# Kernel tuning notes

Hardware: AMD Instinct MI355X
Metric: run time of the kernel (lower is better)

Reference implementation:

```python
import jax, jax.numpy as jnp
import numpy as np

SCALE = 0.5
DROP_P = 0.2

def setup_inputs() -> dict:
    key = jax.random.key(0)
    k1, k2 = jax.random.split(key)
    x1 = jax.random.normal(k1, (8, 2048, 128), dtype=jnp.float32)
    x2 = jax.random.normal(k2, (8, 2048, 128), dtype=jnp.float32)
    return {"x1": x1, "x2": x2}

def reference(x1, x2):
    # scores: [B, M, N] = x1 @ x2^T, scaled by 0.5
    scores = jnp.einsum('bmd,bnd->bmn', x1, x2) * SCALE
    probs = jax.nn.softmax(scores, axis=-1)
    # dropout p=0.2 (training mode in the torch source); fixed key for determinism
    keep = jax.random.bernoulli(jax.random.key(42), 1.0 - DROP_P, probs.shape)
    probs = jnp.where(keep, probs / (1.0 - DROP_P), 0.0)
    # out: [B, M, D] = probs @ x2
    return jnp.einsum('bmn,bnd->bmd', probs, x2)
```

## Files before the change

kernel.cpp:

```cpp
#include <hip/hip_runtime.h>
#include <stdint.h>


typedef __bf16 bf16x8 __attribute__((ext_vector_type(8)));
typedef float f32x4 __attribute__((ext_vector_type(4)));

union FragAB {
  bf16x8 v;
  uint32_t u[4];
};

__device__ __forceinline__ uint32_t rotl32(uint32_t x, uint32_t r) {
  return (x << r) | (x >> (32u - r));
}

__device__ __forceinline__ void threefry2x32_k42(uint32_t in0, uint32_t in1,
                                                 uint32_t& o0, uint32_t& o1) {
  const uint32_t ks0 = 0u;
  const uint32_t ks1 = 42u;
  const uint32_t ks2 = 0x1BD11BDAu ^ 0u ^ 42u;
  uint32_t x0 = in0 + ks0;
  uint32_t x1 = in1 + ks1;
#define TFR(r) { x0 += x1; x1 = rotl32(x1, r); x1 ^= x0; }
  TFR(13u) TFR(15u) TFR(26u) TFR(6u)
  x0 += ks1; x1 += ks2 + 1u;
  TFR(17u) TFR(29u) TFR(16u) TFR(24u)
  x0 += ks2; x1 += ks0 + 2u;
  TFR(13u) TFR(15u) TFR(26u) TFR(6u)
  x0 += ks0; x1 += ks1 + 3u;
  TFR(17u) TFR(29u) TFR(16u) TFR(24u)
  x0 += ks1; x1 += ks2 + 4u;
  TFR(13u) TFR(15u) TFR(26u) TFR(6u)
  x0 += ks2; x1 += ks0 + 5u;
#undef TFR
  o0 = x0; o1 = x1;
}

__device__ __forceinline__ uint32_t pack_bf16(float a, float b) {
  __bf16 ba = (__bf16)a;
  __bf16 bb = (__bf16)b;
  uint32_t ua = (uint32_t)__builtin_bit_cast(uint16_t, ba);
  uint32_t ub = (uint32_t)__builtin_bit_cast(uint16_t, bb);
  return ua | (ub << 16);
}

#define KEEP_LT 3435974144u
#define MBIAS 40.0f

__launch_bounds__(256, 2)
__global__ void attn_kernel(const float* __restrict__ x1,
                            const float* __restrict__ x2,
                            float* __restrict__ out) {
  __shared__ __attribute__((aligned(16))) uint32_t SMEM[4][4800];

  const int tid = threadIdx.x;
  const int wv = __builtin_amdgcn_readfirstlane(tid >> 6);
  const int lane = tid & 63;
  const int l15 = lane & 15;
  const int g = lane >> 4;
  const int b = blockIdx.y;
  const int m0 = blockIdx.x * 32;

  uint32_t* KtW = &SMEM[wv][0];
  uint32_t* VtW = &SMEM[wv][2176];
  uint32_t* PbW = &SMEM[wv][4480];

  const float QSCALE = 0.5f * 1.44269504088896340736f;
  FragAB qf[2][4];
  #pragma unroll
  for (int s = 0; s < 2; ++s) {
    const float* qp_base = x1 + ((size_t)b * 2048 + m0 + s * 16 + l15) * 128;
    #pragma unroll
    for (int c = 0; c < 4; ++c) {
      const float* qp = qp_base + c * 32 + g * 8;
      float4 f0 = *(const float4*)(qp);
      float4 f1 = *(const float4*)(qp + 4);
      qf[s][c].u[0] = pack_bf16(f0.x * QSCALE, f0.y * QSCALE);
      qf[s][c].u[1] = pack_bf16(f0.z * QSCALE, f0.w * QSCALE);
      qf[s][c].u[2] = pack_bf16(f1.x * QSCALE, f1.y * QSCALE);
      qf[s][c].u[3] = pack_bf16(f1.z * QSCALE, f1.w * QSCALE);
    }
  }

  f32x4 o[2][8];
  #pragma unroll
  for (int s = 0; s < 2; ++s)
    #pragma unroll
    for (int dt = 0; dt < 8; ++dt) o[s][dt] = (f32x4){0.f, 0.f, 0.f, 0.f};
  float lsum[2] = {0.f, 0.f};

  uint32_t rb[2];
  #pragma unroll
  for (int s = 0; s < 2; ++s)
    rb[s] = (uint32_t)b * 4194304u +
            (uint32_t)(m0 + s * 16 + l15) * 2048u + (uint32_t)(wv * 512);

  const float4* x2b4 = (const float4*)(x2 + (size_t)b * 2048 * 128);
  const uint32_t permsel = (l15 & 1) ? 0x07060302u : 0x05040100u;

  for (int tile = 0; tile < 16; ++tile) {
    const int n0g = wv * 512 + tile * 32;

    #pragma unroll
    for (int i = 0; i < 16; ++i) {
      int n = 2 * i + (lane >> 5);
      int dq = lane & 31;
      float4 v = x2b4[(size_t)(n0g + n) * 32 + dq];
      uint32_t p0 = pack_bf16(v.x, v.y);
      uint32_t p1 = pack_bf16(v.z, v.w);
      *(uint2*)&KtW[n * 68 + 2 * dq] = make_uint2(p0, p1);
      VtW[dq * 36 + n] = p0;
      VtW[(dq + 32) * 36 + n] = p1;
    }
    asm volatile("s_waitcnt lgkmcnt(0)" ::: "memory");

    f32x4 sa[2][2];
    #pragma unroll
    for (int s = 0; s < 2; ++s)
      #pragma unroll
      for (int t = 0; t < 2; ++t) sa[s][t] = (f32x4){0.f, 0.f, 0.f, 0.f};
    #pragma unroll
    for (int c = 0; c < 4; ++c) {
      FragAB k0, k1;
      uint4 a0 = *(const uint4*)&KtW[l15 * 68 + c * 16 + 4 * g];
      uint4 a1 = *(const uint4*)&KtW[(16 + l15) * 68 + c * 16 + 4 * g];
      k0.u[0] = a0.x; k0.u[1] = a0.y; k0.u[2] = a0.z; k0.u[3] = a0.w;
      k1.u[0] = a1.x; k1.u[1] = a1.y; k1.u[2] = a1.z; k1.u[3] = a1.w;
      sa[0][0] = __builtin_amdgcn_mfma_f32_16x16x32_bf16(k0.v, qf[0][c].v, sa[0][0], 0, 0, 0);
      sa[0][1] = __builtin_amdgcn_mfma_f32_16x16x32_bf16(k1.v, qf[0][c].v, sa[0][1], 0, 0, 0);
      sa[1][0] = __builtin_amdgcn_mfma_f32_16x16x32_bf16(k0.v, qf[1][c].v, sa[1][0], 0, 0, 0);
      sa[1][1] = __builtin_amdgcn_mfma_f32_16x16x32_bf16(k1.v, qf[1][c].v, sa[1][1], 0, 0, 0);
    }

    FragAB pa[2];
    #pragma unroll
    for (int s = 0; s < 2; ++s) {
      #pragma unroll
      for (int t = 0; t < 2; ++t) {
        float p0 = __builtin_amdgcn_exp2f(sa[s][t][0] - MBIAS);
        float p1 = __builtin_amdgcn_exp2f(sa[s][t][1] - MBIAS);
        float p2 = __builtin_amdgcn_exp2f(sa[s][t][2] - MBIAS);
        float p3 = __builtin_amdgcn_exp2f(sa[s][t][3] - MBIAS);
        lsum[s] += (p0 + p1) + (p2 + p3);
        uint32_t ib = rb[s] + (uint32_t)(tile * 32 + t * 16 + 4 * g);
        uint32_t h0, h1, bits;
        threefry2x32_k42(0u, ib + 0u, h0, h1); bits = h0 ^ h1;
        float q0 = (bits < KEEP_LT) ? p0 : 0.0f;
        threefry2x32_k42(0u, ib + 1u, h0, h1); bits = h0 ^ h1;
        float q1 = (bits < KEEP_LT) ? p1 : 0.0f;
        threefry2x32_k42(0u, ib + 2u, h0, h1); bits = h0 ^ h1;
        float q2 = (bits < KEEP_LT) ? p2 : 0.0f;
        threefry2x32_k42(0u, ib + 3u, h0, h1); bits = h0 ^ h1;
        float q3 = (bits < KEEP_LT) ? p3 : 0.0f;
        *(uint2*)&PbW[l15 * 20 + t * 8 + 2 * g] =
            make_uint2(pack_bf16(q0, q1), pack_bf16(q2, q3));
      }
      asm volatile("s_waitcnt lgkmcnt(0)" ::: "memory");
      uint4 pu = *(const uint4*)&PbW[l15 * 20 + 4 * g];
      pa[s].u[0] = pu.x; pa[s].u[1] = pu.y; pa[s].u[2] = pu.z; pa[s].u[3] = pu.w;
    }

    #pragma unroll
    for (int dt = 0; dt < 8; ++dt) {
      int rowp = ((l15 >> 1) & 1) * 32 + 4 * dt + (l15 >> 2);
      const uint32_t* vr = &VtW[rowp * 36 + 8 * g];
      uint4 U0 = *(const uint4*)vr;
      uint4 U1 = *(const uint4*)(vr + 4);
      FragAB vb;
      vb.u[0] = __builtin_amdgcn_perm(U0.y, U0.x, permsel);
      vb.u[1] = __builtin_amdgcn_perm(U0.w, U0.z, permsel);
      vb.u[2] = __builtin_amdgcn_perm(U1.y, U1.x, permsel);
      vb.u[3] = __builtin_amdgcn_perm(U1.w, U1.z, permsel);
      o[0][dt] = __builtin_amdgcn_mfma_f32_16x16x32_bf16(pa[0].v, vb.v, o[0][dt], 0, 0, 0);
      o[1][dt] = __builtin_amdgcn_mfma_f32_16x16x32_bf16(pa[1].v, vb.v, o[1][dt], 0, 0, 0);
    }
  }

  __syncthreads();
  float* EP = (float*)&SMEM[0][0];
  #pragma unroll
  for (int s = 0; s < 2; ++s) {
    #pragma unroll
    for (int dt = 0; dt < 8; ++dt)
      #pragma unroll
      for (int r = 0; r < 4; ++r)
        EP[(((wv * 2 + s) * 8 + dt) * 4 + r) * 64 + lane] = o[s][dt][r];
    EP[16384 + (s * 16 + l15) * 16 + wv * 4 + g] = lsum[s];
  }
  __syncthreads();
  const int s = wv >> 1;
  float scale[4];
  #pragma unroll
  for (int r = 0; r < 4; ++r) {
    const float4* lp = (const float4*)&EP[16384 + (s * 16 + 4 * g + r) * 16];
    float4 A = lp[0], B4 = lp[1], C4 = lp[2], D4 = lp[3];
    float L = ((A.x + A.y) + (A.z + A.w)) + ((B4.x + B4.y) + (B4.z + B4.w)) +
              ((C4.x + C4.y) + (C4.z + C4.w)) + ((D4.x + D4.y) + (D4.z + D4.w));
    scale[r] = 1.0f / (L * 0.8f);
  }
  #pragma unroll
  for (int it = 0; it < 4; ++it) {
    int dt = (wv * 4 + it) & 7;
    #pragma unroll
    for (int r = 0; r < 4; ++r) {
      int base = ((s * 8 + dt) * 4 + r) * 64 + lane;
      float tot = EP[base] + EP[base + 4096] + EP[base + 8192] + EP[base + 12288];
      out[((size_t)b * 2048 + m0 + s * 16 + 4 * g + r) * 128 + dt * 16 + l15] =
          tot * scale[r];
    }
  }
}

extern "C" void kernel_launch(void* const* d_in, const int* in_sizes, int n_in,
                              void* d_out, int out_size, void* d_ws, size_t ws_size,
                              hipStream_t stream) {
  const float* x1 = (const float*)d_in[0];
  const float* x2 = (const float*)d_in[1];
  float* out = (float*)d_out;
  dim3 grid(64, 8, 1);
  dim3 block(256, 1, 1);
  attn_kernel<<<grid, block, 0, stream>>>(x1, x2, out);
}
```

Measured before the change: 155.6 us.

## Halve query rows per block, load K directly from global, raise occupancy

Each block now handles 16 query rows instead of 32, doubling the grid and raising launch bounds to 4 blocks per CU. The K tile is no longer staged in LDS; each wave loads K rows straight from global memory into MFMA fragments. This shrinks LDS use and lets V use a tighter stride. The rotate in the threefry RNG is replaced by alignbit. In exchange, K/V global traffic per query row doubles and the per-tile RNG work is no longer amortized across two query slices.

```diff
diff --git a/kernel.cpp b/kernel.cpp
--- a/kernel.cpp
+++ b/kernel.cpp
@@ -10,9 +10,7 @@
   uint32_t u[4];
 };
 
-__device__ __forceinline__ uint32_t rotl32(uint32_t x, uint32_t r) {
-  return (x << r) | (x >> (32u - r));
-}
+#define ROTL(x, r) __builtin_amdgcn_alignbit((x), (x), 32u - (r))
 
 __device__ __forceinline__ void threefry2x32_k42(uint32_t in0, uint32_t in1,
                                                  uint32_t& o0, uint32_t& o1) {
@@ -21,7 +19,7 @@
   const uint32_t ks2 = 0x1BD11BDAu ^ 0u ^ 42u;
   uint32_t x0 = in0 + ks0;
   uint32_t x1 = in1 + ks1;
-#define TFR(r) { x0 += x1; x1 = rotl32(x1, r); x1 ^= x0; }
+#define TFR(r) { x0 += x1; x1 = ROTL(x1, r); x1 ^= x0; }
   TFR(13u) TFR(15u) TFR(26u) TFR(6u)
   x0 += ks1; x1 += ks2 + 1u;
   TFR(17u) TFR(29u) TFR(16u) TFR(24u)
@@ -47,11 +45,11 @@
 #define KEEP_LT 3435974144u
 #define MBIAS 40.0f
 
-__launch_bounds__(256, 2)
+__launch_bounds__(256, 4)
 __global__ void attn_kernel(const float* __restrict__ x1,
                             const float* __restrict__ x2,
                             float* __restrict__ out) {
-  __shared__ __attribute__((aligned(16))) uint32_t SMEM[4][4800];
+  __shared__ __attribute__((aligned(16))) uint32_t SMEM[4][2496];
 
   const int tid = threadIdx.x;
   const int wv = __builtin_amdgcn_readfirstlane(tid >> 6);
@@ -59,153 +57,143 @@
   const int l15 = lane & 15;
   const int g = lane >> 4;
   const int b = blockIdx.y;
-  const int m0 = blockIdx.x * 32;
-
-  uint32_t* KtW = &SMEM[wv][0];
-  uint32_t* VtW = &SMEM[wv][2176];
-  uint32_t* PbW = &SMEM[wv][4480];
+  const int m0 = blockIdx.x * 16;
+
+  uint32_t* VtW = &SMEM[wv][0];
+  uint32_t* PbW = &SMEM[wv][2176];
+
+  const float* x2b = x2 + (size_t)b * 2048 * 128;
+  const float4* x2b4 = (const float4*)x2b;
 
   const float QSCALE = 0.5f * 1.44269504088896340736f;
-  FragAB qf[2][4];
-  #pragma unroll
-  for (int s = 0; s < 2; ++s) {
-    const float* qp_base = x1 + ((size_t)b * 2048 + m0 + s * 16 + l15) * 128;
+  FragAB qf[4];
+  {
+    const float* qp_base = x1 + ((size_t)b * 2048 + m0 + l15) * 128;
     #pragma unroll
     for (int c = 0; c < 4; ++c) {
       const float* qp = qp_base + c * 32 + g * 8;
       float4 f0 = *(const float4*)(qp);
       float4 f1 = *(const float4*)(qp + 4);
-      qf[s][c].u[0] = pack_bf16(f0.x * QSCALE, f0.y * QSCALE);
-      qf[s][c].u[1] = pack_bf16(f0.z * QSCALE, f0.w * QSCALE);
-      qf[s][c].u[2] = pack_bf16(f1.x * QSCALE, f1.y * QSCALE);
-      qf[s][c].u[3] = pack_bf16(f1.z * QSCALE, f1.w * QSCALE);
-    }
-  }
-
-  f32x4 o[2][8];
-  #pragma unroll
-  for (int s = 0; s < 2; ++s)
-    #pragma unroll
-    for (int dt = 0; dt < 8; ++dt) o[s][dt] = (f32x4){0.f, 0.f, 0.f, 0.f};
-  float lsum[2] = {0.f, 0.f};
-
-  uint32_t rb[2];
-  #pragma unroll
-  for (int s = 0; s < 2; ++s)
-    rb[s] = (uint32_t)b * 4194304u +
-            (uint32_t)(m0 + s * 16 + l15) * 2048u + (uint32_t)(wv * 512);
-
-  const float4* x2b4 = (const float4*)(x2 + (size_t)b * 2048 * 128);
+      qf[c].u[0] = pack_bf16(f0.x * QSCALE, f0.y * QSCALE);
+      qf[c].u[1] = pack_bf16(f0.z * QSCALE, f0.w * QSCALE);
+      qf[c].u[2] = pack_bf16(f1.x * QSCALE, f1.y * QSCALE);
+      qf[c].u[3] = pack_bf16(f1.z * QSCALE, f1.w * QSCALE);
+    }
+  }
+
+  f32x4 o[8];
+  #pragma unroll
+  for (int dt = 0; dt < 8; ++dt) o[dt] = (f32x4){0.f, 0.f, 0.f, 0.f};
+  float lsum = 0.f;
+
+  const uint32_t rb = (uint32_t)b * 4194304u +
+                      (uint32_t)(m0 + l15) * 2048u + (uint32_t)(wv * 512);
+
   const uint32_t permsel = (l15 & 1) ? 0x07060302u : 0x05040100u;
+  const int nrow = lane >> 5;
+  const int dq = lane & 31;
 
   for (int tile = 0; tile < 16; ++tile) {
     const int n0g = wv * 512 + tile * 32;
 
     #pragma unroll
     for (int i = 0; i < 16; ++i) {
-      int n = 2 * i + (lane >> 5);
-      int dq = lane & 31;
+      int n = 2 * i + nrow;
       float4 v = x2b4[(size_t)(n0g + n) * 32 + dq];
-      uint32_t p0 = pack_bf16(v.x, v.y);
-      uint32_t p1 = pack_bf16(v.z, v.w);
-      *(uint2*)&KtW[n * 68 + 2 * dq] = make_uint2(p0, p1);
-      VtW[dq * 36 + n] = p0;
-      VtW[(dq + 32) * 36 + n] = p1;
+      VtW[dq * 34 + n] = pack_bf16(v.x, v.y);
+      VtW[(dq + 32) * 34 + n] = pack_bf16(v.z, v.w);
+    }
+
+    f32x4 sa[2];
+    #pragma unroll
+    for (int t = 0; t < 2; ++t) sa[t] = (f32x4){0.f, 0.f, 0.f, 0.f};
+    #pragma unroll
+    for (int t = 0; t < 2; ++t) {
+      const float* krow = x2b + (size_t)(n0g + t * 16 + l15) * 128 + g * 8;
+      #pragma unroll
+      for (int c = 0; c < 4; ++c) {
+        float4 f0 = *(const float4*)(krow + c * 32);
+        float4 f1 = *(const float4*)(krow + c * 32 + 4);
+        FragAB kf;
+        kf.u[0] = pack_bf16(f0.x, f0.y);
+        kf.u[1] = pack_bf16(f0.z, f0.w);
+        kf.u[2] = pack_bf16(f1.x, f1.y);
+        kf.u[3] = pack_bf16(f1.z, f1.w);
+        sa[t] = __builtin_amdgcn_mfma_f32_16x16x32_bf16(kf.v, qf[c].v, sa[t], 0, 0, 0);
+      }
+    }
+
+    #pragma unroll
+    for (int t = 0; t < 2; ++t) {
+      float p0 = __builtin_amdgcn_exp2f(sa[t][0] - MBIAS);
+      float p1 = __builtin_amdgcn_exp2f(sa[t][1] - MBIAS);
+      float p2 = __builtin_amdgcn_exp2f(sa[t][2] - MBIAS);
+      float p3 = __builtin_amdgcn_exp2f(sa[t][3] - MBIAS);
+      lsum += (p0 + p1) + (p2 + p3);
+      uint32_t ib = rb + (uint32_t)(tile * 32 + t * 16 + 4 * g);
+      uint32_t h0, h1, bits;
+      threefry2x32_k42(0u, ib + 0u, h0, h1); bits = h0 ^ h1;
+      float q0 = (bits < KEEP_LT) ? p0 : 0.0f;
+      threefry2x32_k42(0u, ib + 1u, h0, h1); bits = h0 ^ h1;
+      float q1 = (bits < KEEP_LT) ? p1 : 0.0f;
+      threefry2x32_k42(0u, ib + 2u, h0, h1); bits = h0 ^ h1;
+      float q2 = (bits < KEEP_LT) ? p2 : 0.0f;
+      threefry2x32_k42(0u, ib + 3u, h0, h1); bits = h0 ^ h1;
+      float q3 = (bits < KEEP_LT) ? p3 : 0.0f;
+      *(uint2*)&PbW[l15 * 20 + t * 8 + 2 * g] =
+          make_uint2(pack_bf16(q0, q1), pack_bf16(q2, q3));
     }
     asm volatile("s_waitcnt lgkmcnt(0)" ::: "memory");
 
-    f32x4 sa[2][2];
-    #pragma unroll
-    for (int s = 0; s < 2; ++s)
-      #pragma unroll
-      for (int t = 0; t < 2; ++t) sa[s][t] = (f32x4){0.f, 0.f, 0.f, 0.f};
-    #pragma unroll
-    for (int c = 0; c < 4; ++c) {
-      FragAB k0, k1;
-      uint4 a0 = *(const uint4*)&KtW[l15 * 68 + c * 16 + 4 * g];
-      uint4 a1 = *(const uint4*)&KtW[(16 + l15) * 68 + c * 16 + 4 * g];
-      k0.u[0] = a0.x; k0.u[1] = a0.y; k0.u[2] = a0.z; k0.u[3] = a0.w;
-      k1.u[0] = a1.x; k1.u[1] = a1.y; k1.u[2] = a1.z; k1.u[3] = a1.w;
-      sa[0][0] = __builtin_amdgcn_mfma_f32_16x16x32_bf16(k0.v, qf[0][c].v, sa[0][0], 0, 0, 0);
-      sa[0][1] = __builtin_amdgcn_mfma_f32_16x16x32_bf16(k1.v, qf[0][c].v, sa[0][1], 0, 0, 0);
-      sa[1][0] = __builtin_amdgcn_mfma_f32_16x16x32_bf16(k0.v, qf[1][c].v, sa[1][0], 0, 0, 0);
-      sa[1][1] = __builtin_amdgcn_mfma_f32_16x16x32_bf16(k1.v, qf[1][c].v, sa[1][1], 0, 0, 0);
-    }
-
-    FragAB pa[2];
-    #pragma unroll
-    for (int s = 0; s < 2; ++s) {
-      #pragma unroll
-      for (int t = 0; t < 2; ++t) {
-        float p0 = __builtin_amdgcn_exp2f(sa[s][t][0] - MBIAS);
-        float p1 = __builtin_amdgcn_exp2f(sa[s][t][1] - MBIAS);
-        float p2 = __builtin_amdgcn_exp2f(sa[s][t][2] - MBIAS);
-        float p3 = __builtin_amdgcn_exp2f(sa[s][t][3] - MBIAS);
-        lsum[s] += (p0 + p1) + (p2 + p3);
-        uint32_t ib = rb[s] + (uint32_t)(tile * 32 + t * 16 + 4 * g);
-        uint32_t h0, h1, bits;
-        threefry2x32_k42(0u, ib + 0u, h0, h1); bits = h0 ^ h1;
-        float q0 = (bits < KEEP_LT) ? p0 : 0.0f;
-        threefry2x32_k42(0u, ib + 1u, h0, h1); bits = h0 ^ h1;
-        float q1 = (bits < KEEP_LT) ? p1 : 0.0f;
-        threefry2x32_k42(0u, ib + 2u, h0, h1); bits = h0 ^ h1;
-        float q2 = (bits < KEEP_LT) ? p2 : 0.0f;
-        threefry2x32_k42(0u, ib + 3u, h0, h1); bits = h0 ^ h1;
-        float q3 = (bits < KEEP_LT) ? p3 : 0.0f;
-        *(uint2*)&PbW[l15 * 20 + t * 8 + 2 * g] =
-            make_uint2(pack_bf16(q0, q1), pack_bf16(q2, q3));
-      }
-      asm volatile("s_waitcnt lgkmcnt(0)" ::: "memory");
+    FragAB pa;
+    {
       uint4 pu = *(const uint4*)&PbW[l15 * 20 + 4 * g];
-      pa[s].u[0] = pu.x; pa[s].u[1] = pu.y; pa[s].u[2] = pu.z; pa[s].u[3] = pu.w;
-    }
-
+      pa.u[0] = pu.x; pa.u[1] = pu.y; pa.u[2] = pu.z; pa.u[3] = pu.w;
+    }
     #pragma unroll
     for (int dt = 0; dt < 8; ++dt) {
       int rowp = ((l15 >> 1) & 1) * 32 + 4 * dt + (l15 >> 2);
-      const uint32_t* vr = &VtW[rowp * 36 + 8 * g];
-      uint4 U0 = *(const uint4*)vr;
-      uint4 U1 = *(const uint4*)(vr + 4);
+      const uint32_t* vr = &VtW[rowp * 34 + 8 * g];
+      uint2 w0 = *(const uint2*)(vr);
+      uint2 w1 = *(const uint2*)(vr + 2);
+      uint2 w2 = *(const uint2*)(vr + 4);
+      uint2 w3 = *(const uint2*)(vr + 6);
       FragAB vb;
-      vb.u[0] = __builtin_amdgcn_perm(U0.y, U0.x, permsel);
-      vb.u[1] = __builtin_amdgcn_perm(U0.w, U0.z, permsel);
-      vb.u[2] = __builtin_amdgcn_perm(U1.y, U1.x, permsel);
-      vb.u[3] = __builtin_amdgcn_perm(U1.w, U1.z, permsel);
-      o[0][dt] = __builtin_amdgcn_mfma_f32_16x16x32_bf16(pa[0].v, vb.v, o[0][dt], 0, 0, 0);
-      o[1][dt] = __builtin_amdgcn_mfma_f32_16x16x32_bf16(pa[1].v, vb.v, o[1][dt], 0, 0, 0);
+      vb.u[0] = __builtin_amdgcn_perm(w0.y, w0.x, permsel);
+      vb.u[1] = __builtin_amdgcn_perm(w1.y, w1.x, permsel);
+      vb.u[2] = __builtin_amdgcn_perm(w2.y, w2.x, permsel);
+      vb.u[3] = __builtin_amdgcn_perm(w3.y, w3.x, permsel);
+      o[dt] = __builtin_amdgcn_mfma_f32_16x16x32_bf16(pa.v, vb.v, o[dt], 0, 0, 0);
     }
   }
 
   __syncthreads();
   float* EP = (float*)&SMEM[0][0];
   #pragma unroll
-  for (int s = 0; s < 2; ++s) {
-    #pragma unroll
-    for (int dt = 0; dt < 8; ++dt)
-      #pragma unroll
-      for (int r = 0; r < 4; ++r)
-        EP[(((wv * 2 + s) * 8 + dt) * 4 + r) * 64 + lane] = o[s][dt][r];
-    EP[16384 + (s * 16 + l15) * 16 + wv * 4 + g] = lsum[s];
-  }
+  for (int dt = 0; dt < 8; ++dt)
+    #pragma unroll
+    for (int r = 0; r < 4; ++r)
+      EP[((wv * 8 + dt) * 4 + r) * 64 + lane] = o[dt][r];
+  EP[8192 + l15 * 16 + wv * 4 + g] = lsum;
   __syncthreads();
-  const int s = wv >> 1;
+
   float scale[4];
   #pragma unroll
   for (int r = 0; r < 4; ++r) {
-    const float4* lp = (const float4*)&EP[16384 + (s * 16 + 4 * g + r) * 16];
+    const float4* lp = (const float4*)&EP[8192 + (4 * g + r) * 16];
     float4 A = lp[0], B4 = lp[1], C4 = lp[2], D4 = lp[3];
     float L = ((A.x + A.y) + (A.z + A.w)) + ((B4.x + B4.y) + (B4.z + B4.w)) +
               ((C4.x + C4.y) + (C4.z + C4.w)) + ((D4.x + D4.y) + (D4.z + D4.w));
     scale[r] = 1.0f / (L * 0.8f);
   }
   #pragma unroll
-  for (int it = 0; it < 4; ++it) {
-    int dt = (wv * 4 + it) & 7;
+  for (int it = 0; it < 2; ++it) {
+    int dt = wv * 2 + it;
     #pragma unroll
     for (int r = 0; r < 4; ++r) {
-      int base = ((s * 8 + dt) * 4 + r) * 64 + lane;
-      float tot = EP[base] + EP[base + 4096] + EP[base + 8192] + EP[base + 12288];
-      out[((size_t)b * 2048 + m0 + s * 16 + 4 * g + r) * 128 + dt * 16 + l15] =
+      int base = (dt * 4 + r) * 64 + lane;
+      float tot = EP[base] + EP[base + 2048] + EP[base + 4096] + EP[base + 6144];
+      out[((size_t)b * 2048 + m0 + 4 * g + r) * 128 + dt * 16 + l15] =
           tot * scale[r];
     }
   }
@@ -217,7 +205,7 @@
   const float* x1 = (const float*)d_in[0];
   const float* x2 = (const float*)d_in[1];
   float* out = (float*)d_out;
-  dim3 grid(64, 8, 1);
+  dim3 grid(128, 8, 1);
   dim3 block(256, 1, 1);
   attn_kernel<<<grid, block, 0, stream>>>(x1, x2, out);
 }
```

Result: slower. 269.7 us (+73.3%).

## Precompute dropout masks into LDS and shrink shared memory footprint

Applied to the files above, without the earlier changes.

Threefry dropout bits are now computed in a prologue and packed into per-lane bitmasks in LDS, so the main tile loop only tests bits. Rotation uses alignbit. The K staging buffer is halved by processing the 32-key tile in two 16-row halves, and V and P paddings are tightened. The epilogue is reduced one row-group at a time, which cuts total LDS to allow more resident blocks. The cost is extra prologue latency and possible bank conflicts from the new strides.

```diff
diff --git a/kernel.cpp b/kernel.cpp
--- a/kernel.cpp
+++ b/kernel.cpp
@@ -10,9 +10,7 @@
   uint32_t u[4];
 };
 
-__device__ __forceinline__ uint32_t rotl32(uint32_t x, uint32_t r) {
-  return (x << r) | (x >> (32u - r));
-}
+#define ROTL(x, r) __builtin_amdgcn_alignbit((x), (x), 32u - (r))
 
 __device__ __forceinline__ void threefry2x32_k42(uint32_t in0, uint32_t in1,
                                                  uint32_t& o0, uint32_t& o1) {
@@ -21,7 +19,7 @@
   const uint32_t ks2 = 0x1BD11BDAu ^ 0u ^ 42u;
   uint32_t x0 = in0 + ks0;
   uint32_t x1 = in1 + ks1;
-#define TFR(r) { x0 += x1; x1 = rotl32(x1, r); x1 ^= x0; }
+#define TFR(r) { x0 += x1; x1 = ROTL(x1, r); x1 ^= x0; }
   TFR(13u) TFR(15u) TFR(26u) TFR(6u)
   x0 += ks1; x1 += ks2 + 1u;
   TFR(17u) TFR(29u) TFR(16u) TFR(24u)
@@ -36,6 +34,8 @@
   o0 = x0; o1 = x1;
 }
 
+#define KEEP_LT 3435974144u
+
 __device__ __forceinline__ uint32_t pack_bf16(float a, float b) {
   __bf16 ba = (__bf16)a;
   __bf16 bb = (__bf16)b;
@@ -44,14 +44,13 @@
   return ua | (ub << 16);
 }
 
-#define KEEP_LT 3435974144u
 #define MBIAS 40.0f
 
 __launch_bounds__(256, 2)
 __global__ void attn_kernel(const float* __restrict__ x1,
                             const float* __restrict__ x2,
                             float* __restrict__ out) {
-  __shared__ __attribute__((aligned(16))) uint32_t SMEM[4][4800];
+  __shared__ __attribute__((aligned(16))) uint32_t SMEM[4][4032];
 
   const int tid = threadIdx.x;
   const int wv = __builtin_amdgcn_readfirstlane(tid >> 6);
@@ -62,8 +61,38 @@
   const int m0 = blockIdx.x * 32;
 
   uint32_t* KtW = &SMEM[wv][0];
-  uint32_t* VtW = &SMEM[wv][2176];
-  uint32_t* PbW = &SMEM[wv][4480];
+  uint32_t* VtW = &SMEM[wv][1088];
+  uint32_t* PbW = &SMEM[wv][3264];
+  uint32_t* MkW = &SMEM[wv][3520];
+
+  uint32_t rb[2];
+  #pragma unroll
+  for (int s = 0; s < 2; ++s)
+    rb[s] = (uint32_t)b * 4194304u +
+            (uint32_t)(m0 + s * 16 + l15) * 2048u + (uint32_t)(wv * 512);
+
+  {
+    uint32_t accw = 0;
+    #pragma unroll 1
+    for (int t = 0; t < 16; ++t) {
+      uint32_t cur = 0;
+      #pragma unroll
+      for (int s = 0; s < 2; ++s) {
+        #pragma unroll
+        for (int t2 = 0; t2 < 2; ++t2) {
+          uint32_t ib = rb[s] + (uint32_t)(t * 32 + t2 * 16 + 4 * g);
+          #pragma unroll
+          for (int r = 0; r < 4; ++r) {
+            uint32_t h0, h1;
+            threefry2x32_k42(0u, ib + (uint32_t)r, h0, h1);
+            cur |= (((h0 ^ h1) < KEEP_LT) ? 1u : 0u) << (s * 8 + t2 * 4 + r);
+          }
+        }
+      }
+      if (t & 1) MkW[(t >> 1) * 64 + lane] = accw | (cur << 16);
+      else accw = cur;
+    }
+  }
 
   const float QSCALE = 0.5f * 1.44269504088896340736f;
   FragAB qf[2][4];
@@ -89,47 +118,48 @@
     for (int dt = 0; dt < 8; ++dt) o[s][dt] = (f32x4){0.f, 0.f, 0.f, 0.f};
   float lsum[2] = {0.f, 0.f};
 
-  uint32_t rb[2];
-  #pragma unroll
-  for (int s = 0; s < 2; ++s)
-    rb[s] = (uint32_t)b * 4194304u +
-            (uint32_t)(m0 + s * 16 + l15) * 2048u + (uint32_t)(wv * 512);
-
   const float4* x2b4 = (const float4*)(x2 + (size_t)b * 2048 * 128);
   const uint32_t permsel = (l15 & 1) ? 0x07060302u : 0x05040100u;
-
+  const int nrow = lane >> 5;
+  const int dq = lane & 31;
+
+  uint32_t mwreg = 0;
+
+  #pragma unroll 1
   for (int tile = 0; tile < 16; ++tile) {
     const int n0g = wv * 512 + tile * 32;
 
-    #pragma unroll
-    for (int i = 0; i < 16; ++i) {
-      int n = 2 * i + (lane >> 5);
-      int dq = lane & 31;
-      float4 v = x2b4[(size_t)(n0g + n) * 32 + dq];
-      uint32_t p0 = pack_bf16(v.x, v.y);
-      uint32_t p1 = pack_bf16(v.z, v.w);
-      *(uint2*)&KtW[n * 68 + 2 * dq] = make_uint2(p0, p1);
-      VtW[dq * 36 + n] = p0;
-      VtW[(dq + 32) * 36 + n] = p1;
-    }
-    asm volatile("s_waitcnt lgkmcnt(0)" ::: "memory");
+    if ((tile & 1) == 0)
+      mwreg = MkW[(tile >> 1) * 64 + lane];
+    const uint32_t mhalf = (tile & 1) ? (mwreg >> 16) : (mwreg & 0xFFFFu);
 
     f32x4 sa[2][2];
     #pragma unroll
     for (int s = 0; s < 2; ++s)
       #pragma unroll
       for (int t = 0; t < 2; ++t) sa[s][t] = (f32x4){0.f, 0.f, 0.f, 0.f};
-    #pragma unroll
-    for (int c = 0; c < 4; ++c) {
-      FragAB k0, k1;
-      uint4 a0 = *(const uint4*)&KtW[l15 * 68 + c * 16 + 4 * g];
-      uint4 a1 = *(const uint4*)&KtW[(16 + l15) * 68 + c * 16 + 4 * g];
-      k0.u[0] = a0.x; k0.u[1] = a0.y; k0.u[2] = a0.z; k0.u[3] = a0.w;
-      k1.u[0] = a1.x; k1.u[1] = a1.y; k1.u[2] = a1.z; k1.u[3] = a1.w;
-      sa[0][0] = __builtin_amdgcn_mfma_f32_16x16x32_bf16(k0.v, qf[0][c].v, sa[0][0], 0, 0, 0);
-      sa[0][1] = __builtin_amdgcn_mfma_f32_16x16x32_bf16(k1.v, qf[0][c].v, sa[0][1], 0, 0, 0);
-      sa[1][0] = __builtin_amdgcn_mfma_f32_16x16x32_bf16(k0.v, qf[1][c].v, sa[1][0], 0, 0, 0);
-      sa[1][1] = __builtin_amdgcn_mfma_f32_16x16x32_bf16(k1.v, qf[1][c].v, sa[1][1], 0, 0, 0);
+
+    #pragma unroll
+    for (int h = 0; h < 2; ++h) {
+      #pragma unroll
+      for (int i = 0; i < 8; ++i) {
+        int n = h * 16 + 2 * i + nrow;
+        float4 v = x2b4[(size_t)(n0g + n) * 32 + dq];
+        uint32_t p0 = pack_bf16(v.x, v.y);
+        uint32_t p1 = pack_bf16(v.z, v.w);
+        *(uint2*)&KtW[(2 * i + nrow) * 68 + 2 * dq] = make_uint2(p0, p1);
+        VtW[dq * 34 + n] = p0;
+        VtW[(dq + 32) * 34 + n] = p1;
+      }
+      asm volatile("s_waitcnt lgkmcnt(0)" ::: "memory");
+      #pragma unroll
+      for (int c = 0; c < 4; ++c) {
+        FragAB kf;
+        uint4 kk = *(const uint4*)&KtW[l15 * 68 + c * 16 + 4 * g];
+        kf.u[0] = kk.x; kf.u[1] = kk.y; kf.u[2] = kk.z; kf.u[3] = kk.w;
+        sa[0][h] = __builtin_amdgcn_mfma_f32_16x16x32_bf16(kf.v, qf[0][c].v, sa[0][h], 0, 0, 0);
+        sa[1][h] = __builtin_amdgcn_mfma_f32_16x16x32_bf16(kf.v, qf[1][c].v, sa[1][h], 0, 0, 0);
+      }
     }
 
     FragAB pa[2];
@@ -142,71 +172,68 @@
         float p2 = __builtin_amdgcn_exp2f(sa[s][t][2] - MBIAS);
         float p3 = __builtin_amdgcn_exp2f(sa[s][t][3] - MBIAS);
         lsum[s] += (p0 + p1) + (p2 + p3);
-        uint32_t ib = rb[s] + (uint32_t)(tile * 32 + t * 16 + 4 * g);
-        uint32_t h0, h1, bits;
-        threefry2x32_k42(0u, ib + 0u, h0, h1); bits = h0 ^ h1;
-        float q0 = (bits < KEEP_LT) ? p0 : 0.0f;
-        threefry2x32_k42(0u, ib + 1u, h0, h1); bits = h0 ^ h1;
-        float q1 = (bits < KEEP_LT) ? p1 : 0.0f;
-        threefry2x32_k42(0u, ib + 2u, h0, h1); bits = h0 ^ h1;
-        float q2 = (bits < KEEP_LT) ? p2 : 0.0f;
-        threefry2x32_k42(0u, ib + 3u, h0, h1); bits = h0 ^ h1;
-        float q3 = (bits < KEEP_LT) ? p3 : 0.0f;
-        *(uint2*)&PbW[l15 * 20 + t * 8 + 2 * g] =
+        const int bp = s * 8 + t * 4;
+        float q0 = (mhalf & (1u << (bp + 0))) ? p0 : 0.0f;
+        float q1 = (mhalf & (1u << (bp + 1))) ? p1 : 0.0f;
+        float q2 = (mhalf & (1u << (bp + 2))) ? p2 : 0.0f;
+        float q3 = (mhalf & (1u << (bp + 3))) ? p3 : 0.0f;
+        *(uint2*)&PbW[l15 * 16 + t * 8 + 2 * g] =
             make_uint2(pack_bf16(q0, q1), pack_bf16(q2, q3));
       }
       asm volatile("s_waitcnt lgkmcnt(0)" ::: "memory");
-      uint4 pu = *(const uint4*)&PbW[l15 * 20 + 4 * g];
+      uint4 pu = *(const uint4*)&PbW[l15 * 16 + 4 * g];
       pa[s].u[0] = pu.x; pa[s].u[1] = pu.y; pa[s].u[2] = pu.z; pa[s].u[3] = pu.w;
     }
 
     #pragma unroll
     for (int dt = 0; dt < 8; ++dt) {
       int rowp = ((l15 >> 1) & 1) * 32 + 4 * dt + (l15 >> 2);
-      const uint32_t* vr = &VtW[rowp * 36 + 8 * g];
-      uint4 U0 = *(const uint4*)vr;
-      uint4 U1 = *(const uint4*)(vr + 4);
+      const uint32_t* vr = &VtW[rowp * 34 + 8 * g];
+      uint2 w0 = *(const uint2*)(vr);
+      uint2 w1 = *(const uint2*)(vr + 2);
+      uint2 w2 = *(const uint2*)(vr + 4);
+      uint2 w3 = *(const uint2*)(vr + 6);
       FragAB vb;
-      vb.u[0] = __builtin_amdgcn_perm(U0.y, U0.x, permsel);
-      vb.u[1] = __builtin_amdgcn_perm(U0.w, U0.z, permsel);
-      vb.u[2] = __builtin_amdgcn_perm(U1.y, U1.x, permsel);
-      vb.u[3] = __builtin_amdgcn_perm(U1.w, U1.z, permsel);
+      vb.u[0] = __builtin_amdgcn_perm(w0.y, w0.x, permsel);
+      vb.u[1] = __builtin_amdgcn_perm(w1.y, w1.x, permsel);
+      vb.u[2] = __builtin_amdgcn_perm(w2.y, w2.x, permsel);
+      vb.u[3] = __builtin_amdgcn_perm(w3.y, w3.x, permsel);
       o[0][dt] = __builtin_amdgcn_mfma_f32_16x16x32_bf16(pa[0].v, vb.v, o[0][dt], 0, 0, 0);
       o[1][dt] = __builtin_amdgcn_mfma_f32_16x16x32_bf16(pa[1].v, vb.v, o[1][dt], 0, 0, 0);
     }
   }
 
-  __syncthreads();
   float* EP = (float*)&SMEM[0][0];
-  #pragma unroll
+  #pragma unroll 1
   for (int s = 0; s < 2; ++s) {
+    __syncthreads();
     #pragma unroll
     for (int dt = 0; dt < 8; ++dt)
       #pragma unroll
       for (int r = 0; r < 4; ++r)
-        EP[(((wv * 2 + s) * 8 + dt) * 4 + r) * 64 + lane] = o[s][dt][r];
-    EP[16384 + (s * 16 + l15) * 16 + wv * 4 + g] = lsum[s];
-  }
-  __syncthreads();
-  const int s = wv >> 1;
-  float scale[4];
-  #pragma unroll
-  for (int r = 0; r < 4; ++r) {
-    const float4* lp = (const float4*)&EP[16384 + (s * 16 + 4 * g + r) * 16];
-    float4 A = lp[0], B4 = lp[1], C4 = lp[2], D4 = lp[3];
-    float L = ((A.x + A.y) + (A.z + A.w)) + ((B4.x + B4.y) + (B4.z + B4.w)) +
-              ((C4.x + C4.y) + (C4.z + C4.w)) + ((D4.x + D4.y) + (D4.z + D4.w));
-    scale[r] = 1.0f / (L * 0.8f);
-  }
-  #pragma unroll
-  for (int it = 0; it < 4; ++it) {
-    int dt = (wv * 4 + it) & 7;
+        EP[((wv * 8 + dt) * 4 + r) * 64 + lane] = o[s][dt][r];
+    EP[8192 + l15 * 16 + wv * 4 + g] = lsum[s];
+    __syncthreads();
+
+    float scale[4];
     #pragma unroll
     for (int r = 0; r < 4; ++r) {
-      int base = ((s * 8 + dt) * 4 + r) * 64 + lane;
-      float tot = EP[base] + EP[base + 4096] + EP[base + 8192] + EP[base + 12288];
-      out[((size_t)b * 2048 + m0 + s * 16 + 4 * g + r) * 128 + dt * 16 + l15] =
-          tot * scale[r];
+      const float4* lp = (const float4*)&EP[8192 + (4 * g + r) * 16];
+      float4 A = lp[0], B4 = lp[1], C4 = lp[2], D4 = lp[3];
+      float L = ((A.x + A.y) + (A.z + A.w)) + ((B4.x + B4.y) + (B4.z + B4.w)) +
+                ((C4.x + C4.y) + (C4.z + C4.w)) + ((D4.x + D4.y) + (D4.z + D4.w));
+      scale[r] = 1.0f / (L * 0.8f);
+    }
+    #pragma unroll
+    for (int it = 0; it < 2; ++it) {
+      int dt = wv * 2 + it;
+      #pragma unroll
+      for (int r = 0; r < 4; ++r) {
+        int base = (dt * 4 + r) * 64 + lane;
+        float tot = EP[base] + EP[base + 2048] + EP[base + 4096] + EP[base + 6144];
+        out[((size_t)b * 2048 + m0 + s * 16 + 4 * g + r) * 128 + dt * 16 + l15] =
+            tot * scale[r];
+      }
     }
   }
 }
```

Measured after the change: 180.3 us. +15.8%, slower.
